# Optimization experiments

Measured on AMD Instinct MI355X. Metric: run time of the kernel, lower is better.

Reference implementation:

```python
import jax, jax.numpy as jnp
import numpy as np

ENC_DIM, DEC_DIM, ATT_DIM = 2048, 512, 512


def setup_inputs() -> dict:
    key = jax.random.key(0)
    ks = jax.random.split(key, 8)
    s = lambda d: 1.0 / np.sqrt(d)
    return {
        "encoder_features": jax.random.normal(ks[0], (256, ENC_DIM, 14, 14), jnp.float32),
        "decoder_hidden": jax.random.normal(ks[1], (256, DEC_DIM), jnp.float32),
        "W_enc": jax.random.uniform(ks[2], (ENC_DIM, ATT_DIM), jnp.float32, -s(ENC_DIM), s(ENC_DIM)),
        "b_enc": jax.random.uniform(ks[3], (ATT_DIM,), jnp.float32, -s(ENC_DIM), s(ENC_DIM)),
        "W_dec": jax.random.uniform(ks[4], (DEC_DIM, ATT_DIM), jnp.float32, -s(DEC_DIM), s(DEC_DIM)),
        "b_dec": jax.random.uniform(ks[5], (ATT_DIM,), jnp.float32, -s(DEC_DIM), s(DEC_DIM)),
        "W_full": jax.random.uniform(ks[6], (ATT_DIM, 1), jnp.float32, -s(ATT_DIM), s(ATT_DIM)),
        "b_full": jax.random.uniform(ks[7], (1,), jnp.float32, -s(ATT_DIM), s(ATT_DIM)),
    }


def reference(encoder_features, decoder_hidden, W_enc, b_enc, W_dec, b_dec, W_full, b_full):
    B, C, H, W = encoder_features.shape
    # [B, P, C] with P = H*W pixels
    feats = encoder_features.reshape(B, C, H * W).transpose(0, 2, 1)
    enc_att = jnp.einsum('bpc,ca->bpa', feats, W_enc) + b_enc            # [B,P,A]
    dec_att = decoder_hidden @ W_dec + b_dec                              # [B,A]
    att = jnp.einsum('bpa,a->bp', jax.nn.relu(enc_att + dec_att[:, None, :]), W_full[:, 0]) + b_full[0]
    alpha = jax.nn.softmax(att, axis=1)                                   # [B,P]
    context = jnp.einsum('bpc,bp->bc', feats, alpha)                      # [B,C]
    return (context, alpha)
```

## Files before the change

### kernel.cpp

```cpp
#include <hip/hip_runtime.h>

typedef unsigned short u16;
typedef __bf16 bf16x8 __attribute__((ext_vector_type(8)));
typedef float f32x4 __attribute__((ext_vector_type(4)));

#define B_   256
#define C_   2048
#define P_   196
#define A_   512
#define CP_  (C_ * P_)
#define MTOT (B_ * P_)

#define BM 64
#define BK 32
#define NBLK (MTOT / BM)

__device__ __forceinline__ u16 f2bf(float f) {
    unsigned int x = __float_as_uint(f);
    unsigned int r = (x + 0x7fffu + ((x >> 16) & 1u)) >> 16;
    return (u16)r;
}

__device__ __forceinline__ unsigned long long pack4bf(const float* v) {
    unsigned int lo = (unsigned int)f2bf(v[0]) | ((unsigned int)f2bf(v[1]) << 16);
    unsigned int hi = (unsigned int)f2bf(v[2]) | ((unsigned int)f2bf(v[3]) << 16);
    return (unsigned long long)lo | ((unsigned long long)hi << 32);
}

__device__ __forceinline__ void gl_lds16(const void* g, void* l) {
    __builtin_amdgcn_global_load_lds(
        (const __attribute__((address_space(1))) unsigned int*)g,
        (__attribute__((address_space(3))) unsigned int*)l, 16, 0, 0);
}

#define FENCE() asm volatile("" ::: "memory")
#define BAR_VM(N) asm volatile("s_waitcnt vmcnt(" #N ") lgkmcnt(0)\n\ts_barrier" ::: "memory")

__global__ __launch_bounds__(256) void k_transpose_wenc(const float* __restrict__ W,
                                                        u16* __restrict__ Wt) {
    __shared__ u16 tile[64][65];
    int t  = threadIdx.x;
    int cb = (blockIdx.x & 31) * 64;
    int ab = (blockIdx.x >> 5) * 64;
#pragma unroll
    for (int i = 0; i < 16; ++i) {
        int c = (t >> 6) + i * 4;
        int a = t & 63;
        tile[c][a] = f2bf(W[(size_t)(cb + c) * A_ + ab + a]);
    }
    __syncthreads();
#pragma unroll
    for (int i = 0; i < 16; ++i) {
        int a  = (t >> 6) + i * 4;
        int cl = t & 63;
        Wt[(size_t)(ab + a) * C_ + cb + cl] = tile[cl][a];
    }
}

__global__ __launch_bounds__(512) void k_dec_att(const float* __restrict__ dh,
                                                 const float* __restrict__ Wd,
                                                 const float* __restrict__ bd,
                                                 float* __restrict__ out) {
    __shared__ float hL[512];
    int b = blockIdx.x, t = threadIdx.x;
    hL[t] = dh[b * 512 + t];
    __syncthreads();
    float s = bd[t];
#pragma unroll 8
    for (int k = 0; k < 512; ++k) s = fmaf(hL[k], Wd[k * 512 + t], s);
    out[b * 512 + t] = s;
}

#define GEMM_BODY(KK, P, AV, DO_B, DO_PACK, DO_A, VMN)                               \
  {                                                                                  \
    if (DO_B) {                                                                      \
      const u16* sB = srcB + (size_t)((KK) + 1) * 32;                                \
      gl_lds16(sB,                   &Bs[(P) ^ 1][b_off]);                           \
      gl_lds16(sB + (size_t)16 * C_, &Bs[(P) ^ 1][b_off + 512]);                     \
      gl_lds16(sB + (size_t)32 * C_, &Bs[(P) ^ 1][b_off + 1024]);                    \
      gl_lds16(sB + (size_t)48 * C_, &Bs[(P) ^ 1][b_off + 1536]);                    \
      FENCE();                                                                       \
    }                                                                                \
    bf16x8 bfr[4];                                                                   \
    _Pragma("unroll")                                                                \
    for (int tr = 0; tr < 4; ++tr)                                                   \
      bfr[tr] = *(const bf16x8*)&As[P][tr * 512 + lane * 8];                         \
    _Pragma("unroll")                                                                \
    for (int ta = 0; ta < 4; ++ta) {                                                 \
      bf16x8 afr = *(const bf16x8*)&Bs[P][(wv * 4 + ta) * 512 + lane * 8];           \
      _Pragma("unroll")                                                              \
      for (int tr = 0; tr < 4; ++tr)                                                 \
        acc[ta][tr] = __builtin_amdgcn_mfma_f32_16x16x32_bf16(afr, bfr[tr],          \
                                                              acc[ta][tr], 0, 0, 0); \
    }                                                                                \
    if (DO_PACK)                                                                     \
      *(unsigned long long*)&As[(P) ^ 1][a_off] = pack4bf(AV);                       \
    if (DO_A) {                                                                      \
      const float* sA = srcA + (size_t)((KK) + 3) * BK * P_;                         \
      _Pragma("unroll")                                                              \
      for (int j = 0; j < 4; ++j) AV[j] = sA[j * P_];                                \
      FENCE();                                                                       \
    }                                                                                \
    BAR_VM(VMN);                                                                     \
  }

__global__ __launch_bounds__(512, 4) void k_gemm_att(const float* __restrict__ enc,
                                                     const u16* __restrict__ Wt,
                                                     const float* __restrict__ dec_att,
                                                     const float* __restrict__ benc,
                                                     const float* __restrict__ wfull,
                                                     const float* __restrict__ bfull,
                                                     float* __restrict__ att) {
    __shared__ u16   As[2][4 * 512];
    __shared__ u16   Bs[2][32 * 512];
    __shared__ float decL[2][512];
    __shared__ float wL[512];
    float* att_part = (float*)&As[0][0];

    const int t    = threadIdx.x;
    const int lane = t & 63;
    const int wv   = t >> 6;
    const int l16  = lane & 15;
    const int lq   = lane >> 4;
    const int row0 = blockIdx.x * BM;

    const int b0 = row0 / 196;
    const int b1 = (row0 + BM - 1) / 196;
    decL[0][t] = dec_att[b0 * 512 + t] + benc[t];
    decL[1][t] = dec_att[b1 * 512 + t] + benc[t];
    wL[t] = wfull[t];

    const int kq = t & 7;
    const int pl = t >> 3;
    const int pg = row0 + pl;
    const int bb = pg / 196;
    const int pp = pg - bb * 196;
    const float* srcA = enc + (size_t)bb * CP_ + (size_t)(kq * 4) * P_ + pp;
    const int a_off = (pl >> 4) * 512 + ((pl & 15) + 16 * (kq >> 1)) * 8 + (kq & 1) * 4;

    const u16* srcB  = Wt + (size_t)(wv * 64 + l16) * C_ + lq * 8;
    const int  b_off = (wv * 4) * 512 + lane * 8;

    f32x4 acc[4][4] = {};

    float avT[4], av0[4], av1[4];
#pragma unroll
    for (int j = 0; j < 4; ++j) avT[j] = srcA[(size_t)j * P_];
    gl_lds16(srcB,                   &Bs[0][b_off]);
    gl_lds16(srcB + (size_t)16 * C_, &Bs[0][b_off + 512]);
    gl_lds16(srcB + (size_t)32 * C_, &Bs[0][b_off + 1024]);
    gl_lds16(srcB + (size_t)48 * C_, &Bs[0][b_off + 1536]);
    FENCE();
#pragma unroll
    for (int j = 0; j < 4; ++j) av1[j] = srcA[(size_t)1 * BK * P_ + j * P_];
#pragma unroll
    for (int j = 0; j < 4; ++j) av0[j] = srcA[(size_t)2 * BK * P_ + j * P_];
    FENCE();
    *(unsigned long long*)&As[0][a_off] = pack4bf(avT);
    BAR_VM(8);

#pragma unroll 1
    for (int k = 0; k < 60; k += 2) {
        GEMM_BODY(k,     0, av1, 1, 1, 1, 4);
        GEMM_BODY(k + 1, 1, av0, 1, 1, 1, 4);
    }
    GEMM_BODY(60, 0, av1, 1, 1, 1, 4);
    GEMM_BODY(61, 1, av0, 1, 1, 0, 0);
    GEMM_BODY(62, 0, av1, 1, 1, 0, 0);
    GEMM_BODY(63, 1, av0, 0, 0, 0, 0);

    const int col = l16, quad = lq;
#pragma unroll
    for (int tr = 0; tr < 4; ++tr) {
        int rgl = tr * 16 + col;
        int bi  = (row0 + rgl) / 196 - b0;
        float s = 0.0f;
#pragma unroll
        for (int ta = 0; ta < 4; ++ta)
#pragma unroll
            for (int rr = 0; rr < 4; ++rr) {
                int a_idx = wv * 64 + ta * 16 + quad * 4 + rr;
                float v = acc[ta][tr][rr] + decL[bi][a_idx];
                s = fmaf(fmaxf(v, 0.0f), wL[a_idx], s);
            }
        s += __shfl_xor(s, 16);
        s += __shfl_xor(s, 32);
        if (quad == 0) att_part[wv * 64 + rgl] = s;
    }
    __syncthreads();
    if (t < BM) {
        float s = bfull[0];
#pragma unroll
        for (int w = 0; w < 8; ++w) s += att_part[w * 64 + t];
        att[row0 + t] = s;
    }
}

__global__ __launch_bounds__(64) void k_softmax(const float* __restrict__ att,
                                                float* __restrict__ alpha) {
    int b = blockIdx.x, lane = threadIdx.x;
    const float* a = att + b * P_;
    float v[4];
    float mx = -__builtin_inff();
#pragma unroll
    for (int i = 0; i < 4; ++i) {
        int p = lane + i * 64;
        v[i] = (p < P_) ? a[p] : -__builtin_inff();
        mx = fmaxf(mx, v[i]);
    }
#pragma unroll
    for (int off = 32; off >= 1; off >>= 1) mx = fmaxf(mx, __shfl_xor(mx, off));
    float sum = 0.0f;
#pragma unroll
    for (int i = 0; i < 4; ++i) {
        int p = lane + i * 64;
        float e = (p < P_) ? expf(v[i] - mx) : 0.0f;
        v[i] = e;
        sum += e;
    }
#pragma unroll
    for (int off = 32; off >= 1; off >>= 1) sum += __shfl_xor(sum, off);
    float inv = 1.0f / sum;
#pragma unroll
    for (int i = 0; i < 4; ++i) {
        int p = lane + i * 64;
        if (p < P_) alpha[b * P_ + p] = v[i] * inv;
    }
}

__global__ __launch_bounds__(256) void k_context(const float* __restrict__ enc,
                                                 const float* __restrict__ alpha,
                                                 float* __restrict__ ctx) {
    __shared__ float aL[200];
    int t = threadIdx.x;
    int b = blockIdx.x >> 5;
    int chunk = blockIdx.x & 31;
    if (t < P_) aL[t] = alpha[b * P_ + t];
    __syncthreads();
    int wv = t >> 6, l = t & 63, g = l >> 4, j = l & 15;
    float4 a0 = *(const float4*)&aL[j * 4];
    float4 a1 = *(const float4*)&aL[64 + j * 4];
    float4 a2 = *(const float4*)&aL[128 + j * 4];
    float4 a3 = *(const float4*)&aL[192];
    const float* base = enc + (size_t)b * CP_ + (size_t)(chunk * 64) * P_;
#pragma unroll
    for (int pass = 0; pass < 4; ++pass) {
        int r = wv * 16 + pass * 4 + g;
        const float* row = base + (size_t)r * P_;
        float4 f0 = *(const float4*)(row + j * 4);
        float4 f1 = *(const float4*)(row + 64 + j * 4);
        float4 f2 = *(const float4*)(row + 128 + j * 4);
        float s = f0.x * a0.x + f0.y * a0.y + f0.z * a0.z + f0.w * a0.w;
        s += f1.x * a1.x + f1.y * a1.y + f1.z * a1.z + f1.w * a1.w;
        s += f2.x * a2.x + f2.y * a2.y + f2.z * a2.z + f2.w * a2.w;
        if (j == 0) {
            float4 f3 = *(const float4*)(row + 192);
            s += f3.x * a3.x + f3.y * a3.y + f3.z * a3.z + f3.w * a3.w;
        }
        s += __shfl_xor(s, 1);
        s += __shfl_xor(s, 2);
        s += __shfl_xor(s, 4);
        s += __shfl_xor(s, 8);
        if (j == 0) ctx[(size_t)b * C_ + chunk * 64 + r] = s;
    }
}

extern "C" void kernel_launch(void* const* d_in, const int* in_sizes, int n_in,
                              void* d_out, int out_size, void* d_ws, size_t ws_size,
                              hipStream_t stream) {
    const float* enc   = (const float*)d_in[0];
    const float* dh    = (const float*)d_in[1];
    const float* Wenc  = (const float*)d_in[2];
    const float* benc  = (const float*)d_in[3];
    const float* Wdec  = (const float*)d_in[4];
    const float* bdec  = (const float*)d_in[5];
    const float* wfull = (const float*)d_in[6];
    const float* bfull = (const float*)d_in[7];

    u16*   Wt  = (u16*)d_ws;
    float* dec = (float*)((char*)d_ws + (2u << 20));
    float* att = (float*)((char*)d_ws + (2u << 20) + (512u << 10));

    float* ctx     = (float*)d_out;
    float* alpha_o = ctx + B_ * C_;

    k_transpose_wenc<<<dim3(256), dim3(256), 0, stream>>>(Wenc, Wt);
    k_dec_att<<<dim3(256), dim3(512), 0, stream>>>(dh, Wdec, bdec, dec);
    k_gemm_att<<<dim3(NBLK), dim3(512), 0, stream>>>(enc, Wt, dec, benc,
                                                     wfull, bfull, att);
    k_softmax<<<dim3(256), dim3(64), 0, stream>>>(att, alpha_o);
    k_context<<<dim3(256 * 32), dim3(256), 0, stream>>>(enc, alpha_o, ctx);
}
```

Measured before the change: 920.3 us.

## Double GEMM row tile to 128 with 1024-thread blocks and 2x8 wave grid

Raises the rows per block from 64 to 128 and doubles the block to 1024 threads, arranged as a 2x8 wave grid, so each W_enc tile loaded into LDS is reused across twice as many rows. The A-operand prefetch distance drops from two stages to one, the pack-to-LDS step moves to the start of each stage, and the MFMA section runs under raised wave priority with an explicit sched_barrier before the block barrier. The aim is to halve redundant weight traffic per output row and improve MFMA issue. In exchange, each barrier syncs twice as many waves, the block uses more LDS, and occupancy may drop, while the shorter prefetch may expose more global latency on the encoder loads.

Result: faster. 861.1 us (-6.4%).

```diff
diff --git a/kernel.cpp b/kernel.cpp
--- a/kernel.cpp
+++ b/kernel.cpp
@@ -11,7 +11,7 @@
 #define CP_  (C_ * P_)
 #define MTOT (B_ * P_)
 
-#define BM 64
+#define BM 128
 #define BK 32
 #define NBLK (MTOT / BM)
 
@@ -34,7 +34,6 @@
 }
 
 #define FENCE() asm volatile("" ::: "memory")
-#define BAR_VM(N) asm volatile("s_waitcnt vmcnt(" #N ") lgkmcnt(0)\n\ts_barrier" ::: "memory")
 
 __global__ __launch_bounds__(256) void k_transpose_wenc(const float* __restrict__ W,
                                                         u16* __restrict__ Wt) {
@@ -71,47 +70,50 @@
     out[b * 512 + t] = s;
 }
 
-#define GEMM_BODY(KK, P, AV, DO_B, DO_PACK, DO_A, VMN)                               \
+#define GBODY(KK, P, AVP, AVN, DO_PACK, DO_B, DO_A, VMN)                             \
   {                                                                                  \
+    if (DO_PACK)                                                                     \
+      *(unsigned long long*)&As[(P) ^ 1][a_off] = pack4bf(AVP);                      \
     if (DO_B) {                                                                      \
       const u16* sB = srcB + (size_t)((KK) + 1) * 32;                                \
       gl_lds16(sB,                   &Bs[(P) ^ 1][b_off]);                           \
       gl_lds16(sB + (size_t)16 * C_, &Bs[(P) ^ 1][b_off + 512]);                     \
-      gl_lds16(sB + (size_t)32 * C_, &Bs[(P) ^ 1][b_off + 1024]);                    \
-      gl_lds16(sB + (size_t)48 * C_, &Bs[(P) ^ 1][b_off + 1536]);                    \
       FENCE();                                                                       \
     }                                                                                \
-    bf16x8 bfr[4];                                                                   \
+    if (DO_A) {                                                                      \
+      const float* sA = srcA + (size_t)((KK) + 2) * BK * P_;                         \
+      _Pragma("unroll")                                                              \
+      for (int j = 0; j < 4; ++j) AVN[j] = sA[(size_t)j * P_];                       \
+      FENCE();                                                                       \
+    }                                                                                \
+    bf16x8 bfr[4], afr[4];                                                           \
     _Pragma("unroll")                                                                \
     for (int tr = 0; tr < 4; ++tr)                                                   \
-      bfr[tr] = *(const bf16x8*)&As[P][tr * 512 + lane * 8];                         \
+      bfr[tr] = *(const bf16x8*)&As[P][(wr * 4 + tr) * 512 + lane * 8];              \
     _Pragma("unroll")                                                                \
-    for (int ta = 0; ta < 4; ++ta) {                                                 \
-      bf16x8 afr = *(const bf16x8*)&Bs[P][(wv * 4 + ta) * 512 + lane * 8];           \
+    for (int ta = 0; ta < 4; ++ta)                                                   \
+      afr[ta] = *(const bf16x8*)&Bs[P][(wa * 4 + ta) * 512 + lane * 8];              \
+    __builtin_amdgcn_s_setprio(1);                                                   \
+    _Pragma("unroll")                                                                \
+    for (int ta = 0; ta < 4; ++ta)                                                   \
       _Pragma("unroll")                                                              \
       for (int tr = 0; tr < 4; ++tr)                                                 \
-        acc[ta][tr] = __builtin_amdgcn_mfma_f32_16x16x32_bf16(afr, bfr[tr],          \
+        acc[ta][tr] = __builtin_amdgcn_mfma_f32_16x16x32_bf16(afr[ta], bfr[tr],      \
                                                               acc[ta][tr], 0, 0, 0); \
-    }                                                                                \
-    if (DO_PACK)                                                                     \
-      *(unsigned long long*)&As[(P) ^ 1][a_off] = pack4bf(AV);                       \
-    if (DO_A) {                                                                      \
-      const float* sA = srcA + (size_t)((KK) + 3) * BK * P_;                         \
-      _Pragma("unroll")                                                              \
-      for (int j = 0; j < 4; ++j) AV[j] = sA[j * P_];                                \
-      FENCE();                                                                       \
-    }                                                                                \
-    BAR_VM(VMN);                                                                     \
+    __builtin_amdgcn_s_setprio(0);                                                   \
+    asm volatile("s_waitcnt vmcnt(" #VMN ") lgkmcnt(0)" ::: "memory");               \
+    __builtin_amdgcn_sched_barrier(0);                                               \
+    __builtin_amdgcn_s_barrier();                                                    \
   }
 
-__global__ __launch_bounds__(512, 4) void k_gemm_att(const float* __restrict__ enc,
-                                                     const u16* __restrict__ Wt,
-                                                     const float* __restrict__ dec_att,
-                                                     const float* __restrict__ benc,
-                                                     const float* __restrict__ wfull,
-                                                     const float* __restrict__ bfull,
-                                                     float* __restrict__ att) {
-    __shared__ u16   As[2][4 * 512];
+__global__ __launch_bounds__(1024, 4) void k_gemm_att(const float* __restrict__ enc,
+                                                      const u16* __restrict__ Wt,
+                                                      const float* __restrict__ dec_att,
+                                                      const float* __restrict__ benc,
+                                                      const float* __restrict__ wfull,
+                                                      const float* __restrict__ bfull,
+                                                      float* __restrict__ att) {
+    __shared__ u16   As[2][8 * 512];
     __shared__ u16   Bs[2][32 * 512];
     __shared__ float decL[2][512];
     __shared__ float wL[512];
@@ -126,9 +128,12 @@
 
     const int b0 = row0 / 196;
     const int b1 = (row0 + BM - 1) / 196;
-    decL[0][t] = dec_att[b0 * 512 + t] + benc[t];
-    decL[1][t] = dec_att[b1 * 512 + t] + benc[t];
-    wL[t] = wfull[t];
+    if (t < 512) {
+        decL[0][t] = dec_att[b0 * 512 + t] + benc[t];
+        wL[t] = wfull[t];
+    } else {
+        decL[1][t - 512] = dec_att[b1 * 512 + (t - 512)] + benc[t - 512];
+    }
 
     const int kq = t & 7;
     const int pl = t >> 3;
@@ -138,60 +143,59 @@
     const float* srcA = enc + (size_t)bb * CP_ + (size_t)(kq * 4) * P_ + pp;
     const int a_off = (pl >> 4) * 512 + ((pl & 15) + 16 * (kq >> 1)) * 8 + (kq & 1) * 4;
 
-    const u16* srcB  = Wt + (size_t)(wv * 64 + l16) * C_ + lq * 8;
-    const int  b_off = (wv * 4) * 512 + lane * 8;
+    const u16* srcB  = Wt + (size_t)(wv * 2 * 16 + l16) * C_ + lq * 8;
+    const int  b_off = (wv * 2) * 512 + lane * 8;
+
+    const int wr = wv & 1;
+    const int wa = wv >> 1;
 
     f32x4 acc[4][4] = {};
-
-    float avT[4], av0[4], av1[4];
-#pragma unroll
-    for (int j = 0; j < 4; ++j) avT[j] = srcA[(size_t)j * P_];
+    float av0[4], av1[4];
+
+#pragma unroll
+    for (int j = 0; j < 4; ++j) av0[j] = srcA[(size_t)j * P_];
+    *(unsigned long long*)&As[0][a_off] = pack4bf(av0);
     gl_lds16(srcB,                   &Bs[0][b_off]);
     gl_lds16(srcB + (size_t)16 * C_, &Bs[0][b_off + 512]);
-    gl_lds16(srcB + (size_t)32 * C_, &Bs[0][b_off + 1024]);
-    gl_lds16(srcB + (size_t)48 * C_, &Bs[0][b_off + 1536]);
     FENCE();
 #pragma unroll
-    for (int j = 0; j < 4; ++j) av1[j] = srcA[(size_t)1 * BK * P_ + j * P_];
-#pragma unroll
-    for (int j = 0; j < 4; ++j) av0[j] = srcA[(size_t)2 * BK * P_ + j * P_];
+    for (int j = 0; j < 4; ++j) av0[j] = srcA[(size_t)BK * P_ + (size_t)j * P_];
     FENCE();
-    *(unsigned long long*)&As[0][a_off] = pack4bf(avT);
-    BAR_VM(8);
+    asm volatile("s_waitcnt vmcnt(4) lgkmcnt(0)" ::: "memory");
+    __builtin_amdgcn_sched_barrier(0);
+    __builtin_amdgcn_s_barrier();
 
 #pragma unroll 1
-    for (int k = 0; k < 60; k += 2) {
-        GEMM_BODY(k,     0, av1, 1, 1, 1, 4);
-        GEMM_BODY(k + 1, 1, av0, 1, 1, 1, 4);
-    }
-    GEMM_BODY(60, 0, av1, 1, 1, 1, 4);
-    GEMM_BODY(61, 1, av0, 1, 1, 0, 0);
-    GEMM_BODY(62, 0, av1, 1, 1, 0, 0);
-    GEMM_BODY(63, 1, av0, 0, 0, 0, 0);
+    for (int k = 0; k < 62; k += 2) {
+        GBODY(k,     0, av0, av1, 1, 1, 1, 4);
+        GBODY(k + 1, 1, av1, av0, 1, 1, 1, 4);
+    }
+    GBODY(62, 0, av0, av1, 1, 1, 0, 0);
+    GBODY(63, 1, av1, av0, 0, 0, 0, 0);
 
     const int col = l16, quad = lq;
 #pragma unroll
     for (int tr = 0; tr < 4; ++tr) {
-        int rgl = tr * 16 + col;
+        int rgl = wr * 64 + tr * 16 + col;
         int bi  = (row0 + rgl) / 196 - b0;
         float s = 0.0f;
 #pragma unroll
         for (int ta = 0; ta < 4; ++ta)
 #pragma unroll
             for (int rr = 0; rr < 4; ++rr) {
-                int a_idx = wv * 64 + ta * 16 + quad * 4 + rr;
+                int a_idx = wa * 64 + ta * 16 + quad * 4 + rr;
                 float v = acc[ta][tr][rr] + decL[bi][a_idx];
                 s = fmaf(fmaxf(v, 0.0f), wL[a_idx], s);
             }
         s += __shfl_xor(s, 16);
         s += __shfl_xor(s, 32);
-        if (quad == 0) att_part[wv * 64 + rgl] = s;
+        if (quad == 0) att_part[wa * 128 + rgl] = s;
     }
     __syncthreads();
     if (t < BM) {
         float s = bfull[0];
 #pragma unroll
-        for (int w = 0; w < 8; ++w) s += att_part[w * 64 + t];
+        for (int w = 0; w < 8; ++w) s += att_part[w * 128 + t];
         att[row0 + t] = s;
     }
 }
@@ -286,8 +290,8 @@
 
     k_transpose_wenc<<<dim3(256), dim3(256), 0, stream>>>(Wenc, Wt);
     k_dec_att<<<dim3(256), dim3(512), 0, stream>>>(dh, Wdec, bdec, dec);
-    k_gemm_att<<<dim3(NBLK), dim3(512), 0, stream>>>(enc, Wt, dec, benc,
-                                                     wfull, bfull, att);
+    k_gemm_att<<<dim3(NBLK), dim3(1024), 0, stream>>>(enc, Wt, dec, benc,
+                                                      wfull, bfull, att);
     k_softmax<<<dim3(256), dim3(64), 0, stream>>>(att, alpha_o);
     k_context<<<dim3(256 * 32), dim3(256), 0, stream>>>(enc, alpha_o, ctx);
 }
```
